# Performance work log

Measured on AMD Instinct MI355X. Metric: run time of the kernel, lower is better.

Reference implementation:

```python
import jax, jax.numpy as jnp
import numpy as np
from jax import lax

D_MODEL = 1024
D_INNER = 2 * D_MODEL  # expand=2
D_CONV = 4
BATCH = 4
SEQ = 4096


def setup_inputs() -> dict:
    key = jax.random.key(0)
    ks = jax.random.split(key, 10)
    s = 0.02
    return {
        "x": jax.random.normal(ks[0], (BATCH, SEQ, D_MODEL), jnp.float32),
        "in_proj_w": jax.random.normal(ks[1], (2 * D_INNER, D_MODEL), jnp.float32) * s,
        "in_proj_b": jnp.zeros((2 * D_INNER,), jnp.float32),
        "conv_w": jax.random.normal(ks[2], (D_INNER, 1, D_CONV), jnp.float32) * s,
        "conv_b": jnp.zeros((D_INNER,), jnp.float32),
        "dt_w": jax.random.normal(ks[3], (D_INNER, D_INNER), jnp.float32) * s,
        "dt_b": jnp.zeros((D_INNER,), jnp.float32),
        "b_w": jax.random.normal(ks[4], (D_INNER, D_INNER), jnp.float32) * s,
        "c_w": jax.random.normal(ks[5], (D_INNER, D_INNER), jnp.float32) * s,
        "A_log": jax.random.normal(ks[6], (D_INNER,), jnp.float32) * 0.02 - 2.0,
        "D_param": jnp.ones((D_INNER,), jnp.float32),
        "out_w": jax.random.normal(ks[7], (D_MODEL, D_INNER), jnp.float32) * s,
        "out_b": jnp.zeros((D_MODEL,), jnp.float32),
    }


def _mixer(x, in_proj_w, in_proj_b, conv_w, conv_b, dt_w, dt_b,
           b_w, c_w, A_log, D_param, out_w, out_b):
    B, L, _ = x.shape
    # input projection -> split into x/z branches
    xz = jnp.einsum("bld,ed->ble", x, in_proj_w) + in_proj_b
    x_branch, z_branch = jnp.split(xz, 2, axis=-1)  # each [B, L, d_inner]

    # causal depthwise conv1d (padding=d_conv-1 on the left == torch pad then [:L])
    u = jnp.transpose(x_branch, (0, 2, 1))  # [B, d_inner, L]
    u = lax.conv_general_dilated(
        u, conv_w,
        window_strides=(1,),
        padding=[(D_CONV - 1, 0)],
        dimension_numbers=("NCH", "OIH", "NCH"),
        feature_group_count=D_INNER,
    ) + conv_b[None, :, None]
    u = jnp.transpose(u, (0, 2, 1))  # [B, L, d_inner]
    u = jax.nn.silu(u)

    dt = jax.nn.softplus(jnp.einsum("bld,ed->ble", u, dt_w) + dt_b) + 1e-4
    B_t = jnp.tanh(jnp.einsum("bld,ed->ble", u, b_w))
    C_t = jnp.tanh(jnp.einsum("bld,ed->ble", u, c_w))

    A = jnp.exp(A_log)  # [d_inner]
    decay = jnp.exp(-dt * A)          # [B, L, d_inner]
    inc = (1.0 - decay) * B_t * u     # [B, L, d_inner]

    # linear recurrence: state_t = decay_t * state_{t-1} + inc_t
    def step(state, xs):
        d_t, i_t = xs
        state = d_t * state + i_t
        return state, state

    init = jnp.zeros((B, D_INNER), x.dtype)
    _, states = lax.scan(step, init,
                         (jnp.transpose(decay, (1, 0, 2)),
                          jnp.transpose(inc, (1, 0, 2))))  # [L, B, d_inner]
    states = jnp.transpose(states, (1, 0, 2))  # [B, L, d_inner]

    y = C_t * states + D_param * u
    y = y * jax.nn.sigmoid(z_branch)  # SiLU-style gate
    # dropout is identity in eval mode
    return jnp.einsum("ble,de->bld", y, out_w) + out_b


def reference(x, in_proj_w, in_proj_b, conv_w, conv_b, dt_w, dt_b,
              b_w, c_w, A_log, D_param, out_w, out_b):
    return _mixer(x, in_proj_w, in_proj_b, conv_w, conv_b, dt_w, dt_b,
                  b_w, c_w, A_log, D_param, out_w, out_b)
```

## Files before the change

kernel.cpp:

```cpp
#include <hip/hip_runtime.h>
#include <math.h>
#include <stdint.h>


#define BATCH 4
#define SEQ 4096
#define DMODEL 1024
#define DINNER 2048
#define CLS 32

typedef __bf16 bf16_t;
typedef __bf16 bf16x8 __attribute__((ext_vector_type(8)));
typedef float f32x4 __attribute__((ext_vector_type(4)));
typedef unsigned short ushort_t;
typedef unsigned short u16x4 __attribute__((ext_vector_type(4)));

enum { EP_F32 = 0, EP_BF = 1, EP_SIG = 2, EP_DT = 3, EP_TANH = 4 };

__device__ __forceinline__ void gload_lds16(const void* g, void* l) {
    __builtin_amdgcn_global_load_lds(
        (const __attribute__((address_space(1))) void*)g,
        (__attribute__((address_space(3))) void*)l, 16, 0, 0);
}

__device__ __forceinline__ ushort_t f2bf(float f) {
    union { float f; uint32_t u; } c; c.f = f;
    uint32_t u = c.u;
    u += 0x7fffu + ((u >> 16) & 1u);
    return (ushort_t)(u >> 16);
}
__device__ __forceinline__ float bf2f(ushort_t h) {
    union { uint32_t u; float f; } c; c.u = (uint32_t)h << 16;
    return c.f;
}
__device__ __forceinline__ float tanh_exact(float v) {
    v = fminf(fmaxf(v, -15.f), 15.f);
    float e = __expf(2.f * v);
    return (e - 1.f) / (e + 1.f);
}
__device__ __forceinline__ float tanh_poly(float v) {
    float v2 = v * v;
    float t = v * (1.f - v2 * (0.33333333f - 0.13333333f * v2));
    if (__builtin_expect(fabsf(v) > 0.25f, 0)) t = tanh_exact(v);
    return t;
}
__device__ __forceinline__ float softplus_poly(float v) {
    float v2 = v * v;
    float s = 0.69314718f + 0.5f * v + v2 * (0.125f - 0.0052083333f * v2);
    if (__builtin_expect(fabsf(v) > 0.25f, 0))
        s = fmaxf(v, 0.f) + __logf(1.f + __expf(-fabsf(v)));
    return s;
}

#define GBK 64

__global__ __launch_bounds__(256) void gemm_bf16_ep(
    const bf16_t* __restrict__ A, const bf16_t* __restrict__ W,
    const float* __restrict__ bias,
    float* __restrict__ Cf, ushort_t* __restrict__ T0,
    const float* __restrict__ alogp,
    int K, int Nout, int Lc, int a_bstride, int a_l0,
    int c_bstride, int c_l0, int mode)
{
    __shared__ __align__(16) bf16_t smem[128 * 128];
    bf16_t* sA = smem;
    bf16_t* sB = smem + 128 * GBK;
    const int tid = threadIdx.x;
    const int lane = tid & 63;
    const int wid = tid >> 6;
    const int wm = wid >> 1, wn = wid & 1;
    const int n0 = blockIdx.x * 128;
    const int m0 = blockIdx.y * 128;
    const int bb = m0 / Lc;
    const int lb = m0 - bb * Lc;
    const bf16_t* Abase = A + ((size_t)bb * a_bstride + a_l0 + lb) * K;
    const bf16_t* Wbase = W + (size_t)n0 * K;

    int st_row[4], st_sc[4], st_ofs[4];
#pragma unroll
    for (int i = 0; i < 4; ++i) {
        int ofs = tid * 16 + i * 4096;
        int r = ofs >> 7;
        int c16 = (ofs >> 4) & 7;
        st_ofs[i] = ofs;
        st_row[i] = r;
        st_sc[i] = (c16 ^ (r & 7)) << 3;
    }

    f32x4 acc[4][4];
#pragma unroll
    for (int i = 0; i < 4; ++i)
#pragma unroll
        for (int j = 0; j < 4; ++j) acc[i][j] = f32x4{0.f, 0.f, 0.f, 0.f};

    for (int k0 = 0; k0 < K; k0 += GBK) {
#pragma unroll
        for (int i = 0; i < 4; ++i) {
            gload_lds16(Abase + (size_t)st_row[i] * K + k0 + st_sc[i],
                        (char*)sA + st_ofs[i]);
            gload_lds16(Wbase + (size_t)st_row[i] * K + k0 + st_sc[i],
                        (char*)sB + st_ofs[i]);
        }
        __syncthreads();
#pragma unroll
        for (int ks = 0; ks < 2; ++ks) {
            bf16x8 av[4], bv[4];
#pragma unroll
            for (int mi = 0; mi < 4; ++mi) {
                int row = wm * 64 + mi * 16 + (lane & 15);
                int cb = (ks * 64 + ((lane >> 4) << 4)) ^ ((row & 7) << 4);
                av[mi] = *(const bf16x8*)((const char*)sA + row * 128 + cb);
            }
#pragma unroll
            for (int ni = 0; ni < 4; ++ni) {
                int row = wn * 64 + ni * 16 + (lane & 15);
                int cb = (ks * 64 + ((lane >> 4) << 4)) ^ ((row & 7) << 4);
                bv[ni] = *(const bf16x8*)((const char*)sB + row * 128 + cb);
            }
#pragma unroll
            for (int mi = 0; mi < 4; ++mi)
#pragma unroll
                for (int ni = 0; ni < 4; ++ni)
                    acc[mi][ni] = __builtin_amdgcn_mfma_f32_16x16x32_bf16(
                        av[mi], bv[ni], acc[mi][ni], 0, 0, 0);
        }
        __syncthreads();
    }

    const size_t rowbase = (size_t)bb * c_bstride + c_l0 + lb;
    if (mode == EP_F32) {
#pragma unroll
        for (int ni = 0; ni < 4; ++ni) {
            const int coll = wn * 64 + ni * 16 + (lane & 15);
            const float bv = bias ? bias[n0 + coll] : 0.f;
#pragma unroll
            for (int mi = 0; mi < 4; ++mi) {
#pragma unroll
                for (int r4 = 0; r4 < 4; ++r4) {
                    const int rowl = wm * 64 + mi * 16 + ((lane >> 4) << 2) + r4;
                    Cf[(rowbase + rowl) * (size_t)Nout + n0 + coll] =
                        acc[mi][ni][r4] + bv;
                }
            }
        }
    } else {
        ushort_t* sm = (ushort_t*)smem;
#pragma unroll
        for (int ni = 0; ni < 4; ++ni) {
            const int coll = wn * 64 + ni * 16 + (lane & 15);
            const float bv = bias ? bias[n0 + coll] : 0.f;
            const float Ae = (mode == EP_DT) ? __expf(alogp[n0 + coll]) : 0.f;
#pragma unroll
            for (int mi = 0; mi < 4; ++mi) {
#pragma unroll
                for (int r4 = 0; r4 < 4; ++r4) {
                    const int rowl = wm * 64 + mi * 16 + ((lane >> 4) << 2) + r4;
                    float v = acc[mi][ni][r4] + bv;
                    ushort_t o;
                    if (mode == EP_BF)       o = f2bf(v);
                    else if (mode == EP_SIG) o = f2bf(1.f / (1.f + __expf(-v)));
                    else if (mode == EP_DT)
                        o = f2bf(__expf(-(softplus_poly(v) + 1e-4f) * Ae));
                    else                     o = f2bf(tanh_poly(v));
                    sm[rowl * 128 + coll] = o;
                }
            }
        }
        __syncthreads();
#pragma unroll
        for (int it = 0; it < 8; ++it) {
            const int e = tid * 8 + it * 2048;
            const int row = e >> 7;
            const int col = e & 127;
            int4 vv = *(const int4*)(sm + e);
            *(int4*)(T0 + (rowbase + row) * (size_t)Nout + n0 + col) = vv;
        }
    }
}

__global__ __launch_bounds__(256) void cvt_bf16_k(
    const float4* __restrict__ in, ushort4* __restrict__ out, int n4)
{
    for (int i = blockIdx.x * 256 + threadIdx.x; i < n4; i += gridDim.x * 256) {
        float4 v = in[i];
        ushort4 o;
        o.x = f2bf(v.x); o.y = f2bf(v.y); o.z = f2bf(v.z); o.w = f2bf(v.w);
        out[i] = o;
    }
}

__global__ __launch_bounds__(256) void conv_silu_bf(
    const ushort_t* __restrict__ xb, const ushort_t* __restrict__ tailb,
    const float* __restrict__ cw, const float* __restrict__ cb,
    ushort_t* __restrict__ ubf, int Lc, int l0, size_t total)
{
    for (size_t idx = (size_t)blockIdx.x * 256 + threadIdx.x; idx < total;
         idx += (size_t)gridDim.x * 256) {
        int e = (int)(idx % DINNER);
        size_t r = idx / DINNER;
        int lp = (int)(r % Lc);
        int b  = (int)(r / Lc);
        float4 w = *(const float4*)(cw + (size_t)e * 4);
        float s = cb[e];
        const ushort_t* xbase = xb + (size_t)b * Lc * DINNER + e;
        if (lp >= 3) {
            s += bf2f(xbase[(size_t)(lp - 3) * DINNER]) * w.x
               + bf2f(xbase[(size_t)(lp - 2) * DINNER]) * w.y
               + bf2f(xbase[(size_t)(lp - 1) * DINNER]) * w.z
               + bf2f(xbase[(size_t)lp * DINNER]) * w.w;
        } else {
            const float ws4[4] = {w.x, w.y, w.z, w.w};
            const ushort_t* tbase = tailb + (size_t)b * 3 * DINNER + e;
#pragma unroll
            for (int j = 0; j < 4; ++j) {
                int ls = lp - 3 + j;
                float v;
                if (ls >= 0)            v = bf2f(xbase[(size_t)ls * DINNER]);
                else if (l0 + ls >= 0)  v = bf2f(tbase[(size_t)(3 + ls) * DINNER]);
                else                    v = 0.f;
                s += v * ws4[j];
            }
        }
        ubf[idx] = f2bf(s / (1.f + __expf(-s)));
    }
}

__global__ __launch_bounds__(256) void tail_update_bf(
    const ushort_t* __restrict__ xb, ushort_t* __restrict__ tailb, int Lc)
{
    int idx = blockIdx.x * 256 + threadIdx.x;
    if (idx >= BATCH * 3 * DINNER) return;
    int e = idx % DINNER;
    int j = (idx / DINNER) % 3;
    int b = idx / (3 * DINNER);
    tailb[idx] = xb[((size_t)b * Lc + Lc - 3 + j) * DINNER + e];
}

__global__ __launch_bounds__(256) void scan1_v4(
    const ushort_t* __restrict__ dec, const ushort_t* __restrict__ bt,
    const ushort_t* __restrict__ ub,
    float* __restrict__ P, float* __restrict__ S, int Lc, int nsub)
{
    int t = blockIdx.x * 256 + threadIdx.x;
    int e = (t & 511) << 2;
    int rest = t >> 9;
    int c = rest % nsub;
    int b = rest / nsub;
    size_t off = ((size_t)b * Lc + (size_t)c * CLS) * DINNER + e;
    float p[4] = {1.f, 1.f, 1.f, 1.f};
    float s[4] = {0.f, 0.f, 0.f, 0.f};
    for (int t0 = 0; t0 < CLS; ++t0) {
        size_t o = off + (size_t)t0 * DINNER;
        u16x4 d4 = *(const u16x4*)(dec + o);
        u16x4 b4 = *(const u16x4*)(bt + o);
        u16x4 u4 = *(const u16x4*)(ub + o);
#pragma unroll
        for (int j = 0; j < 4; ++j) {
            float d = bf2f(d4[j]);
            float inc = (1.f - d) * bf2f(b4[j]) * bf2f(u4[j]);
            s[j] = d * s[j] + inc;
            p[j] *= d;
        }
    }
    size_t po = ((size_t)b * nsub + c) * DINNER + e;
    *(float4*)(P + po) = float4{p[0], p[1], p[2], p[3]};
    *(float4*)(S + po) = float4{s[0], s[1], s[2], s[3]};
}

__global__ __launch_bounds__(256) void scan_p2(
    float* __restrict__ P, float* __restrict__ S,
    float* __restrict__ carry, int nsub, int first)
{
    int idx = blockIdx.x * 256 + threadIdx.x;
    int e = idx % DINNER;
    int b = idx / DINNER;
    float cv = first ? 0.f : carry[idx];
    for (int c = 0; c < nsub; ++c) {
        size_t o = ((size_t)b * nsub + c) * DINNER + e;
        float p = P[o], s = S[o];
        P[o] = cv;
        cv = p * cv + s;
    }
    carry[idx] = cv;
}

__global__ __launch_bounds__(256) void p3y_v4(
    const ushort_t* __restrict__ dec, ushort_t* __restrict__ bty,
    const ushort_t* __restrict__ ct, const ushort_t* __restrict__ ub,
    const ushort_t* __restrict__ sg, const float* __restrict__ Dp,
    const float* __restrict__ Pc, int Lc, int nsub)
{
    int t = blockIdx.x * 256 + threadIdx.x;
    int e = (t & 511) << 2;
    int rest = t >> 9;
    int c = rest % nsub;
    int b = rest / nsub;
    size_t off = ((size_t)b * Lc + (size_t)c * CLS) * DINNER + e;
    size_t po = ((size_t)b * nsub + c) * DINNER + e;
    float4 stv = *(const float4*)(Pc + po);
    float4 Dv  = *(const float4*)(Dp + e);
    float st[4] = {stv.x, stv.y, stv.z, stv.w};
    float D4[4] = {Dv.x, Dv.y, Dv.z, Dv.w};
    for (int t0 = 0; t0 < CLS; ++t0) {
        size_t o = off + (size_t)t0 * DINNER;
        u16x4 d4 = *(const u16x4*)(dec + o);
        u16x4 b4 = *(const u16x4*)(bty + o);
        u16x4 c4 = *(const u16x4*)(ct + o);
        u16x4 u4 = *(const u16x4*)(ub + o);
        u16x4 g4 = *(const u16x4*)(sg + o);
        u16x4 y4;
#pragma unroll
        for (int j = 0; j < 4; ++j) {
            float d = bf2f(d4[j]);
            float u = bf2f(u4[j]);
            float inc = (1.f - d) * bf2f(b4[j]) * u;
            st[j] = d * st[j] + inc;
            float y = bf2f(c4[j]) * st[j] + D4[j] * u;
            y4[j] = f2bf(y * bf2f(g4[j]));
        }
        *(u16x4*)(bty + o) = y4;
    }
}

extern "C" void kernel_launch(void* const* d_in, const int* in_sizes, int n_in,
                              void* d_out, int out_size, void* d_ws, size_t ws_size,
                              hipStream_t stream)
{
    const float* x    = (const float*)d_in[0];
    const float* ipw  = (const float*)d_in[1];
    const float* ipb  = (const float*)d_in[2];
    const float* cw   = (const float*)d_in[3];
    const float* cb   = (const float*)d_in[4];
    const float* dtw  = (const float*)d_in[5];
    const float* dtb  = (const float*)d_in[6];
    const float* bw   = (const float*)d_in[7];
    const float* cwt  = (const float*)d_in[8];
    const float* alog = (const float*)d_in[9];
    const float* dpar = (const float*)d_in[10];
    const float* ow   = (const float*)d_in[11];
    const float* ob   = (const float*)d_in[12];
    float* out = (float*)d_out;

    const size_t XN   = (size_t)BATCH * SEQ * DMODEL;
    const size_t WIP  = (size_t)2 * DINNER * DMODEL;
    const size_t WSQ  = (size_t)DINNER * DINNER;
    const size_t WOUT = (size_t)DMODEL * DINNER;
    const size_t const_bytes = 2 * (XN + WIP + 3 * WSQ + WOUT);

    const int cands[6] = {4096, 2048, 1024, 512, 256, 128};
    int Lc = 128;
    for (int i = 0; i < 6; ++i) {
        size_t NBe = (size_t)BATCH * cands[i] * DINNER;
        size_t need = const_bytes
                    + 5 * NBe * 2
                    + (size_t)BATCH * 3 * DINNER * 2
                    + (size_t)BATCH * DINNER * 4
                    + 2 * (size_t)BATCH * (cands[i] / CLS) * DINNER * 4
                    + 1024;
        if (need <= ws_size) { Lc = cands[i]; break; }
    }
    const int nsub = Lc / CLS;
    const size_t NBe = (size_t)BATCH * Lc * DINNER;

    char* p = (char*)d_ws;
    ushort_t* xbf   = (ushort_t*)p; p += XN * 2;
    ushort_t* ipwbf = (ushort_t*)p; p += WIP * 2;
    ushort_t* dtwbf = (ushort_t*)p; p += WSQ * 2;
    ushort_t* bwbf  = (ushort_t*)p; p += WSQ * 2;
    ushort_t* cwtbf = (ushort_t*)p; p += WSQ * 2;
    ushort_t* owbf  = (ushort_t*)p; p += WOUT * 2;
    ushort_t* S1 = (ushort_t*)p; p += NBe * 2;
    ushort_t* S2 = (ushort_t*)p; p += NBe * 2;
    ushort_t* S3 = (ushort_t*)p; p += NBe * 2;
    ushort_t* S4 = (ushort_t*)p; p += NBe * 2;
    ushort_t* S5 = (ushort_t*)p; p += NBe * 2;
    ushort_t* tailb = (ushort_t*)p; p += (size_t)BATCH * 3 * DINNER * 2;
    float* carry = (float*)p; p += (size_t)BATCH * DINNER * 4;
    float* Pb    = (float*)p; p += (size_t)BATCH * nsub * DINNER * 4;
    float* Sb    = (float*)p;

    const dim3 blk(256);
    const int M = BATCH * Lc;
    const dim3 gSq(DINNER / 128, M / 128);
    const dim3 gOut(DMODEL / 128, M / 128);
    const int pwBlocks = (int)(((NBe + 255) / 256 < 4096) ? (NBe + 255) / 256 : 4096);
    const int scanBlocks = BATCH * nsub * 2;

    auto cvt = [&](const float* in, ushort_t* outp, size_t n) {
        int n4 = (int)(n / 4);
        int g = n4 / 256 < 2048 ? (n4 + 255) / 256 : 2048;
        cvt_bf16_k<<<g, blk, 0, stream>>>((const float4*)in, (ushort4*)outp, n4);
    };
    cvt(x, xbf, XN);
    cvt(ipw, ipwbf, WIP);
    cvt(dtw, dtwbf, WSQ);
    cvt(bw, bwbf, WSQ);
    cvt(cwt, cwtbf, WSQ);
    cvt(ow, owbf, WOUT);

    const int nchunks = SEQ / Lc;
    for (int c = 0; c < nchunks; ++c) {
        const int l0 = c * Lc;
        gemm_bf16_ep<<<gSq, blk, 0, stream>>>(
            (const bf16_t*)xbf, (const bf16_t*)ipwbf, ipb,
            nullptr, S1, nullptr,
            DMODEL, DINNER, Lc, SEQ, l0, Lc, 0, EP_BF);
        gemm_bf16_ep<<<gSq, blk, 0, stream>>>(
            (const bf16_t*)xbf, (const bf16_t*)(ipwbf + (size_t)DINNER * DMODEL),
            ipb + DINNER, nullptr, S5, nullptr,
            DMODEL, DINNER, Lc, SEQ, l0, Lc, 0, EP_SIG);
        conv_silu_bf<<<pwBlocks, blk, 0, stream>>>(S1, tailb, cw, cb, S2, Lc, l0, NBe);
        if (nchunks > 1)
            tail_update_bf<<<BATCH * 3 * DINNER / 256, blk, 0, stream>>>(S1, tailb, Lc);
        gemm_bf16_ep<<<gSq, blk, 0, stream>>>(
            (const bf16_t*)S2, (const bf16_t*)dtwbf, dtb,
            nullptr, S3, alog,
            DINNER, DINNER, Lc, Lc, 0, Lc, 0, EP_DT);
        gemm_bf16_ep<<<gSq, blk, 0, stream>>>(
            (const bf16_t*)S2, (const bf16_t*)bwbf, nullptr,
            nullptr, S4, nullptr,
            DINNER, DINNER, Lc, Lc, 0, Lc, 0, EP_TANH);
        gemm_bf16_ep<<<gSq, blk, 0, stream>>>(
            (const bf16_t*)S2, (const bf16_t*)cwtbf, nullptr,
            nullptr, S1, nullptr,
            DINNER, DINNER, Lc, Lc, 0, Lc, 0, EP_TANH);
        scan1_v4<<<scanBlocks, blk, 0, stream>>>(S3, S4, S2, Pb, Sb, Lc, nsub);
        scan_p2<<<BATCH * DINNER / 256, blk, 0, stream>>>(Pb, Sb, carry, nsub, c == 0);
        p3y_v4<<<scanBlocks, blk, 0, stream>>>(S3, S4, S1, S2, S5, dpar, Pb, Lc, nsub);
        gemm_bf16_ep<<<gOut, blk, 0, stream>>>(
            (const bf16_t*)S4, (const bf16_t*)owbf, ob,
            out, nullptr, nullptr,
            DINNER, DMODEL, Lc, Lc, 0, SEQ, l0, EP_F32);
    }
}
```

Baseline: 1.122 ms.

## Batch dt/B/C GEMMs via grid z, fuse gate into z-projection epilogue

Merges the three square GEMMs (dt, B, C) into one launch, using blockIdx.z to select a concatenated weight and output buffer. The z-branch projection now runs after the scan and applies sigmoid(z) to y in its epilogue, so the p3y kernel no longer reads a gate buffer and one full bf16 intermediate is dropped. It also adds an XOR swizzle to the LDS staging in the epilogue to reduce bank conflicts. The aims are fewer launches, better occupancy and less memory traffic, while the gate epilogue adds an uncoalesced global read per element.

```diff
diff --git a/kernel.cpp b/kernel.cpp
--- a/kernel.cpp
+++ b/kernel.cpp
@@ -15,7 +15,7 @@
 typedef unsigned short ushort_t;
 typedef unsigned short u16x4 __attribute__((ext_vector_type(4)));
 
-enum { EP_F32 = 0, EP_BF = 1, EP_SIG = 2, EP_DT = 3, EP_TANH = 4 };
+enum { EP_F32 = 0, EP_BF = 1, EP_DBC = 2, EP_GATE = 3 };
 
 __device__ __forceinline__ void gload_lds16(const void* g, void* l) {
     __builtin_amdgcn_global_load_lds(
@@ -58,6 +58,7 @@
     const bf16_t* __restrict__ A, const bf16_t* __restrict__ W,
     const float* __restrict__ bias,
     float* __restrict__ Cf, ushort_t* __restrict__ T0,
+    ushort_t* __restrict__ T1, ushort_t* __restrict__ T2,
     const float* __restrict__ alogp,
     int K, int Nout, int Lc, int a_bstride, int a_l0,
     int c_bstride, int c_l0, int mode)
@@ -65,6 +66,10 @@
     __shared__ __align__(16) bf16_t smem[128 * 128];
     bf16_t* sA = smem;
     bf16_t* sB = smem + 128 * GBK;
+    const int wz = blockIdx.z;
+    const bf16_t* Wmat = W + (size_t)wz * Nout * K;
+    ushort_t* Tz = (wz == 0) ? T0 : (wz == 1 ? T1 : T2);
+
     const int tid = threadIdx.x;
     const int lane = tid & 63;
     const int wid = tid >> 6;
@@ -74,7 +79,7 @@
     const int bb = m0 / Lc;
     const int lb = m0 - bb * Lc;
     const bf16_t* Abase = A + ((size_t)bb * a_bstride + a_l0 + lb) * K;
-    const bf16_t* Wbase = W + (size_t)n0 * K;
+    const bf16_t* Wbase = Wmat + (size_t)n0 * K;
 
     int st_row[4], st_sc[4], st_ofs[4];
 #pragma unroll
@@ -148,8 +153,12 @@
 #pragma unroll
         for (int ni = 0; ni < 4; ++ni) {
             const int coll = wn * 64 + ni * 16 + (lane & 15);
-            const float bv = bias ? bias[n0 + coll] : 0.f;
-            const float Ae = (mode == EP_DT) ? __expf(alogp[n0 + coll]) : 0.f;
+            const int colg = n0 + coll;
+            float bv = 0.f, Ae = 0.f;
+            if (mode == EP_BF || mode == EP_GATE) bv = bias[colg];
+            else if (mode == EP_DBC && wz == 0) {
+                bv = bias[colg]; Ae = __expf(alogp[colg]);
+            }
 #pragma unroll
             for (int mi = 0; mi < 4; ++mi) {
 #pragma unroll
@@ -157,23 +166,30 @@
                     const int rowl = wm * 64 + mi * 16 + ((lane >> 4) << 2) + r4;
                     float v = acc[mi][ni][r4] + bv;
                     ushort_t o;
-                    if (mode == EP_BF)       o = f2bf(v);
-                    else if (mode == EP_SIG) o = f2bf(1.f / (1.f + __expf(-v)));
-                    else if (mode == EP_DT)
-                        o = f2bf(__expf(-(softplus_poly(v) + 1e-4f) * Ae));
-                    else                     o = f2bf(tanh_poly(v));
-                    sm[rowl * 128 + coll] = o;
+                    if (mode == EP_BF) {
+                        o = f2bf(v);
+                    } else if (mode == EP_GATE) {
+                        const size_t off = (rowbase + rowl) * (size_t)Nout + colg;
+                        o = f2bf(bf2f(Tz[off]) / (1.f + __expf(-v)));
+                    } else {
+                        if (wz == 0)
+                            o = f2bf(__expf(-(softplus_poly(v) + 1e-4f) * Ae));
+                        else
+                            o = f2bf(tanh_poly(v));
+                    }
+                    const int sbyte = rowl * 256 + ((coll * 2) ^ ((rowl & 7) << 4));
+                    *(ushort_t*)((char*)sm + sbyte) = o;
                 }
             }
         }
         __syncthreads();
 #pragma unroll
         for (int it = 0; it < 8; ++it) {
-            const int e = tid * 8 + it * 2048;
-            const int row = e >> 7;
-            const int col = e & 127;
-            int4 vv = *(const int4*)(sm + e);
-            *(int4*)(T0 + (rowbase + row) * (size_t)Nout + n0 + col) = vv;
+            const int b0 = tid * 16 + it * 4096;
+            const int row = b0 >> 8;
+            const int src = (b0 & ~255) | ((b0 & 255) ^ ((row & 7) << 4));
+            int4 vv = *(const int4*)((const char*)sm + src);
+            *(int4*)(Tz + (rowbase + row) * (size_t)Nout + n0 + ((b0 & 255) >> 1)) = vv;
         }
     }
 }
@@ -287,8 +303,8 @@
 __global__ __launch_bounds__(256) void p3y_v4(
     const ushort_t* __restrict__ dec, ushort_t* __restrict__ bty,
     const ushort_t* __restrict__ ct, const ushort_t* __restrict__ ub,
-    const ushort_t* __restrict__ sg, const float* __restrict__ Dp,
-    const float* __restrict__ Pc, int Lc, int nsub)
+    const float* __restrict__ Dp, const float* __restrict__ Pc,
+    int Lc, int nsub)
 {
     int t = blockIdx.x * 256 + threadIdx.x;
     int e = (t & 511) << 2;
@@ -307,7 +323,6 @@
         u16x4 b4 = *(const u16x4*)(bty + o);
         u16x4 c4 = *(const u16x4*)(ct + o);
         u16x4 u4 = *(const u16x4*)(ub + o);
-        u16x4 g4 = *(const u16x4*)(sg + o);
         u16x4 y4;
 #pragma unroll
         for (int j = 0; j < 4; ++j) {
@@ -315,8 +330,7 @@
             float u = bf2f(u4[j]);
             float inc = (1.f - d) * bf2f(b4[j]) * u;
             st[j] = d * st[j] + inc;
-            float y = bf2f(c4[j]) * st[j] + D4[j] * u;
-            y4[j] = f2bf(y * bf2f(g4[j]));
+            y4[j] = f2bf(bf2f(c4[j]) * st[j] + D4[j] * u);
         }
         *(u16x4*)(bty + o) = y4;
     }
@@ -352,7 +366,7 @@
     for (int i = 0; i < 6; ++i) {
         size_t NBe = (size_t)BATCH * cands[i] * DINNER;
         size_t need = const_bytes
-                    + 5 * NBe * 2
+                    + 4 * NBe * 2
                     + (size_t)BATCH * 3 * DINNER * 2
                     + (size_t)BATCH * DINNER * 4
                     + 2 * (size_t)BATCH * (cands[i] / CLS) * DINNER * 4
@@ -365,15 +379,12 @@
     char* p = (char*)d_ws;
     ushort_t* xbf   = (ushort_t*)p; p += XN * 2;
     ushort_t* ipwbf = (ushort_t*)p; p += WIP * 2;
-    ushort_t* dtwbf = (ushort_t*)p; p += WSQ * 2;
-    ushort_t* bwbf  = (ushort_t*)p; p += WSQ * 2;
-    ushort_t* cwtbf = (ushort_t*)p; p += WSQ * 2;
+    ushort_t* wcat  = (ushort_t*)p; p += 3 * WSQ * 2;
     ushort_t* owbf  = (ushort_t*)p; p += WOUT * 2;
     ushort_t* S1 = (ushort_t*)p; p += NBe * 2;
     ushort_t* S2 = (ushort_t*)p; p += NBe * 2;
     ushort_t* S3 = (ushort_t*)p; p += NBe * 2;
     ushort_t* S4 = (ushort_t*)p; p += NBe * 2;
-    ushort_t* S5 = (ushort_t*)p; p += NBe * 2;
     ushort_t* tailb = (ushort_t*)p; p += (size_t)BATCH * 3 * DINNER * 2;
     float* carry = (float*)p; p += (size_t)BATCH * DINNER * 4;
     float* Pb    = (float*)p; p += (size_t)BATCH * nsub * DINNER * 4;
@@ -381,8 +392,9 @@
 
     const dim3 blk(256);
     const int M = BATCH * Lc;
-    const dim3 gSq(DINNER / 128, M / 128);
-    const dim3 gOut(DMODEL / 128, M / 128);
+    const dim3 gSq(DINNER / 128, M / 128, 1);
+    const dim3 gDBC(DINNER / 128, M / 128, 3);
+    const dim3 gOut(DMODEL / 128, M / 128, 1);
     const int pwBlocks = (int)(((NBe + 255) / 256 < 4096) ? (NBe + 255) / 256 : 4096);
     const int scanBlocks = BATCH * nsub * 2;
 
@@ -393,9 +405,9 @@
     };
     cvt(x, xbf, XN);
     cvt(ipw, ipwbf, WIP);
-    cvt(dtw, dtwbf, WSQ);
-    cvt(bw, bwbf, WSQ);
-    cvt(cwt, cwtbf, WSQ);
+    cvt(dtw, wcat, WSQ);
+    cvt(bw, wcat + WSQ, WSQ);
+    cvt(cwt, wcat + 2 * WSQ, WSQ);
     cvt(ow, owbf, WOUT);
 
     const int nchunks = SEQ / Lc;
@@ -403,33 +415,25 @@
         const int l0 = c * Lc;
         gemm_bf16_ep<<<gSq, blk, 0, stream>>>(
             (const bf16_t*)xbf, (const bf16_t*)ipwbf, ipb,
-            nullptr, S1, nullptr,
+            nullptr, S1, nullptr, nullptr, nullptr,
             DMODEL, DINNER, Lc, SEQ, l0, Lc, 0, EP_BF);
-        gemm_bf16_ep<<<gSq, blk, 0, stream>>>(
-            (const bf16_t*)xbf, (const bf16_t*)(ipwbf + (size_t)DINNER * DMODEL),
-            ipb + DINNER, nullptr, S5, nullptr,
-            DMODEL, DINNER, Lc, SEQ, l0, Lc, 0, EP_SIG);
         conv_silu_bf<<<pwBlocks, blk, 0, stream>>>(S1, tailb, cw, cb, S2, Lc, l0, NBe);
         if (nchunks > 1)
             tail_update_bf<<<BATCH * 3 * DINNER / 256, blk, 0, stream>>>(S1, tailb, Lc);
-        gemm_bf16_ep<<<gSq, blk, 0, stream>>>(
-            (const bf16_t*)S2, (const bf16_t*)dtwbf, dtb,
-            nullptr, S3, alog,
-            DINNER, DINNER, Lc, Lc, 0, Lc, 0, EP_DT);
-        gemm_bf16_ep<<<gSq, blk, 0, stream>>>(
-            (const bf16_t*)S2, (const bf16_t*)bwbf, nullptr,
-            nullptr, S4, nullptr,
-            DINNER, DINNER, Lc, Lc, 0, Lc, 0, EP_TANH);
-        gemm_bf16_ep<<<gSq, blk, 0, stream>>>(
-            (const bf16_t*)S2, (const bf16_t*)cwtbf, nullptr,
-            nullptr, S1, nullptr,
-            DINNER, DINNER, Lc, Lc, 0, Lc, 0, EP_TANH);
+        gemm_bf16_ep<<<gDBC, blk, 0, stream>>>(
+            (const bf16_t*)S2, (const bf16_t*)wcat, dtb,
+            nullptr, S3, S4, S1, alog,
+            DINNER, DINNER, Lc, Lc, 0, Lc, 0, EP_DBC);
         scan1_v4<<<scanBlocks, blk, 0, stream>>>(S3, S4, S2, Pb, Sb, Lc, nsub);
         scan_p2<<<BATCH * DINNER / 256, blk, 0, stream>>>(Pb, Sb, carry, nsub, c == 0);
-        p3y_v4<<<scanBlocks, blk, 0, stream>>>(S3, S4, S1, S2, S5, dpar, Pb, Lc, nsub);
+        p3y_v4<<<scanBlocks, blk, 0, stream>>>(S3, S4, S1, S2, dpar, Pb, Lc, nsub);
+        gemm_bf16_ep<<<gSq, blk, 0, stream>>>(
+            (const bf16_t*)xbf, (const bf16_t*)(ipwbf + (size_t)DINNER * DMODEL),
+            ipb + DINNER, nullptr, S4, nullptr, nullptr, nullptr,
+            DMODEL, DINNER, Lc, SEQ, l0, Lc, 0, EP_GATE);
         gemm_bf16_ep<<<gOut, blk, 0, stream>>>(
             (const bf16_t*)S4, (const bf16_t*)owbf, ob,
-            out, nullptr, nullptr,
+            out, nullptr, nullptr, nullptr, nullptr,
             DINNER, DMODEL, Lc, Lc, 0, SEQ, l0, EP_F32);
     }
 }
```

Result: no change. 1.137 ms (+1.4%).
